# Optimization experiments

Hardware: AMD Instinct MI355X
Metric: run time of the kernel (lower is better)

The kernel has to match this reference:

```python
import jax, jax.numpy as jnp
import numpy as np

BS, D = 8192, 1024


def setup_inputs() -> dict:
    key = jax.random.key(0)
    k1, k2, k3, k4 = jax.random.split(key, 4)
    return {
        "z": jax.random.normal(k1, (BS, D), dtype=jnp.float32),
        "w": jax.random.normal(k2, (BS, D), dtype=jnp.float32),
        "u": jax.random.normal(k3, (BS, D), dtype=jnp.float32),
        "b": jax.random.normal(k4, (BS,), dtype=jnp.float32),
    }


def reference(z, w, u, b):
    # --- get_batch_corrected_u ---
    wu = jnp.sum(w * u, axis=1)                      # [bs]
    m = -1.0 + jax.nn.softplus(wu)                   # [bs]
    # NOTE: original divides by sqrt of GLOBAL sum over all of w (no axis)
    w_norm = jnp.sqrt(jnp.sum(w ** 2))               # scalar
    u_hat = u + ((m - wu)[:, None] * w) / w_norm     # [bs, d]

    # --- forward transform: diag(tanh(wTz+b)) @ u  ==  tanh(...)[:,None]*u ---
    inner = jnp.sum(w * z, axis=1) + b               # [bs]
    z_new = z + jnp.tanh(inner)[:, None] * u_hat     # [bs, d]

    # --- det_jcb evaluated with UPDATED z (as in the original code) ---
    inner2 = jnp.sum(w * z_new, axis=1) + b          # [bs]
    h_prime = 1.0 - jnp.tanh(inner2) ** 2            # [bs]
    psi_dot_u = h_prime * jnp.sum(u_hat * w, axis=1) # [bs]
    log_det = jnp.log(jnp.abs(1.0 + psi_dot_u))      # [bs]
    return z_new, log_det
```

## Files before the change

kernel.cpp:

```cpp
#include <hip/hip_runtime.h>
#include <math.h>

#define BS   8192
#define D    1024
#define NBLK 512
#define RPB  16
#define F4R  4

typedef float floatx4 __attribute__((ext_vector_type(4)));
typedef unsigned long long u64;

__global__ __launch_bounds__(512, 4) void planar512(
    const float* __restrict__ z, const float* __restrict__ w,
    const float* __restrict__ u, const float* __restrict__ b,
    float* __restrict__ zout, float* __restrict__ ldout,
    u64* __restrict__ slots, unsigned int* __restrict__ epoch)
{
    const int t    = threadIdx.x;
    const int wv   = t >> 6;
    const int l    = t & 63;
    const int row0 = blockIdx.x * RPB + wv * 2;

    const unsigned int e1 =
        __hip_atomic_load(epoch, __ATOMIC_RELAXED, __HIP_MEMORY_SCOPE_AGENT)
        + 1u;

    float4 wr[2][F4R];
    float  w2_s[2];
    float  w2acc = 0.f;
#pragma unroll
    for (int r = 0; r < 2; ++r) {
        const float4* w4 = (const float4*)w + (size_t)(row0 + r) * (D / 4);
        float w2 = 0.f;
#pragma unroll
        for (int k = 0; k < F4R; ++k) {
            const float4 a = w4[l + (k << 6)];
            wr[r][k] = a;
            w2 += a.x*a.x + a.y*a.y + a.z*a.z + a.w*a.w;
        }
#pragma unroll
        for (int off = 32; off > 0; off >>= 1) w2 += __shfl_xor(w2, off, 64);
        w2_s[r] = w2;
        w2acc  += w2;
    }
    float brow[2];
#pragma unroll
    for (int r = 0; r < 2; ++r) brow[r] = b[row0 + r];

    __shared__ float sw[8], sg[8];
    if (l == 0) sw[wv] = w2acc;
    __syncthreads();
    if (t == 0) {
        float p = 0.f;
#pragma unroll
        for (int i = 0; i < 8; ++i) p += sw[i];
        const u64 word = ((u64)e1 << 32) | (u64)__float_as_uint(p);
        __hip_atomic_store(&slots[blockIdx.x], word, __ATOMIC_RELAXED,
                           __HIP_MEMORY_SCOPE_AGENT);
    }

    float4 vr[2][F4R];
    float  wu_s[2], in_s[2], th_s[2];
#pragma unroll
    for (int r = 0; r < 2; ++r) {
        const int row = row0 + r;
        const float4* z4 = (const float4*)z + (size_t)row * (D / 4);
        const float4* u4 = (const float4*)u + (size_t)row * (D / 4);
        float4 zv[F4R], uv[F4R];
#pragma unroll
        for (int k = 0; k < F4R; ++k) {
            zv[k] = z4[l + (k << 6)];
            uv[k] = u4[l + (k << 6)];
        }
        float wu = 0.f, wz = 0.f;
#pragma unroll
        for (int k = 0; k < F4R; ++k) {
            const float4 a = wr[r][k];
            wu += a.x*uv[k].x + a.y*uv[k].y + a.z*uv[k].z + a.w*uv[k].w;
            wz += a.x*zv[k].x + a.y*zv[k].y + a.z*zv[k].z + a.w*zv[k].w;
        }
#pragma unroll
        for (int off = 32; off > 0; off >>= 1) {
            wu += __shfl_xor(wu, off, 64);
            wz += __shfl_xor(wz, off, 64);
        }
        const float inner = wz + brow[r];
        const float tnh   = tanhf(inner);
#pragma unroll
        for (int k = 0; k < F4R; ++k) {
            vr[r][k].x = fmaf(tnh, uv[k].x, zv[k].x);
            vr[r][k].y = fmaf(tnh, uv[k].y, zv[k].y);
            vr[r][k].z = fmaf(tnh, uv[k].z, zv[k].z);
            vr[r][k].w = fmaf(tnh, uv[k].w, zv[k].w);
        }
        wu_s[r] = wu; in_s[r] = inner; th_s[r] = tnh;
    }

    u64 a0;
    for (;;) {
        a0 = __hip_atomic_load(&slots[t], __ATOMIC_RELAXED,
                               __HIP_MEMORY_SCOPE_AGENT);
        if ((unsigned int)(a0 >> 32) == e1) break;
        __builtin_amdgcn_s_sleep(4);
    }
    float gs = __uint_as_float((unsigned int)a0);
#pragma unroll
    for (int off = 32; off > 0; off >>= 1) gs += __shfl_xor(gs, off, 64);
    if (l == 0) sg[wv] = gs;
    __syncthreads();
    float gw2 = 0.f;
#pragma unroll
    for (int i = 0; i < 8; ++i) gw2 += sg[i];
    const float wnrm = sqrtf(gw2);

    if (blockIdx.x == 0 && t == 0)
        __hip_atomic_store(epoch, e1, __ATOMIC_RELEASE,
                           __HIP_MEMORY_SCOPE_AGENT);

#pragma unroll
    for (int r = 0; r < 2; ++r) {
        const int   row  = row0 + r;
        const float wu   = wu_s[r];
        const float sp   = (wu > 0.f) ? (wu + log1pf(expf(-wu)))
                                      : log1pf(expf(wu));
        const float coef = (-1.f + sp - wu) / wnrm;
        const float tc   = th_s[r] * coef;
        floatx4* o4 = (floatx4*)zout + (size_t)row * (D / 4);
#pragma unroll
        for (int k = 0; k < F4R; ++k) {
            floatx4 o;
            o.x = fmaf(tc, wr[r][k].x, vr[r][k].x);
            o.y = fmaf(tc, wr[r][k].y, vr[r][k].y);
            o.z = fmaf(tc, wr[r][k].z, vr[r][k].z);
            o.w = fmaf(tc, wr[r][k].w, vr[r][k].w);
            __builtin_nontemporal_store(o, o4 + l + (k << 6));
        }
        if (l == 0) {
            const float s      = fmaf(coef, w2_s[r], wu);
            const float inner2 = fmaf(th_s[r], s, in_s[r]);
            const float th2    = tanhf(inner2);
            const float hp     = 1.f - th2 * th2;
            ldout[row] = logf(fabsf(fmaf(hp, s, 1.f)));
        }
    }
}

__global__ __launch_bounds__(256, 2) void planar256(
    const float* __restrict__ z, const float* __restrict__ w,
    const float* __restrict__ u, const float* __restrict__ b,
    float* __restrict__ zout, float* __restrict__ ldout,
    u64* __restrict__ slots, unsigned int* __restrict__ epoch)
{
    const int t    = threadIdx.x;
    const int wv   = t >> 6;
    const int l    = t & 63;
    const int row0 = blockIdx.x * RPB + wv * 4;

    __shared__ unsigned int s_e;
    __shared__ float sw[4], sg[4];
    if (t == 0)
        s_e = __hip_atomic_load(epoch, __ATOMIC_RELAXED,
                                __HIP_MEMORY_SCOPE_AGENT);

    float4 wr[4][F4R];
    float  w2_s[4];
    float  w2acc = 0.f;
#pragma unroll
    for (int r = 0; r < 4; ++r) {
        const float4* w4 = (const float4*)w + (size_t)(row0 + r) * (D / 4);
        float w2 = 0.f;
#pragma unroll
        for (int k = 0; k < F4R; ++k) {
            const float4 a = w4[l + (k << 6)];
            wr[r][k] = a;
            w2 += a.x*a.x + a.y*a.y + a.z*a.z + a.w*a.w;
        }
#pragma unroll
        for (int off = 32; off > 0; off >>= 1) w2 += __shfl_xor(w2, off, 64);
        w2_s[r] = w2;
        w2acc  += w2;
    }
    if (l == 0) sw[wv] = w2acc;
    __syncthreads();
    const unsigned int e1 = s_e + 1u;
    if (t == 0) {
        const float p = sw[0] + sw[1] + sw[2] + sw[3];
        const u64 word = ((u64)e1 << 32) | (u64)__float_as_uint(p);
        __hip_atomic_store(&slots[blockIdx.x], word, __ATOMIC_RELAXED,
                           __HIP_MEMORY_SCOPE_AGENT);
    }

    float4 vr[4][F4R];
    float  wu_s[4], in_s[4], th_s[4];
#pragma unroll
    for (int r = 0; r < 4; ++r) {
        const int row = row0 + r;
        const float4* z4 = (const float4*)z + (size_t)row * (D / 4);
        const float4* u4 = (const float4*)u + (size_t)row * (D / 4);
        float4 zv[F4R], uv[F4R];
#pragma unroll
        for (int k = 0; k < F4R; ++k) {
            zv[k] = z4[l + (k << 6)];
            uv[k] = u4[l + (k << 6)];
        }
        float wu = 0.f, wz = 0.f;
#pragma unroll
        for (int k = 0; k < F4R; ++k) {
            const float4 a = wr[r][k];
            wu += a.x*uv[k].x + a.y*uv[k].y + a.z*uv[k].z + a.w*uv[k].w;
            wz += a.x*zv[k].x + a.y*zv[k].y + a.z*zv[k].z + a.w*zv[k].w;
        }
#pragma unroll
        for (int off = 32; off > 0; off >>= 1) {
            wu += __shfl_xor(wu, off, 64);
            wz += __shfl_xor(wz, off, 64);
        }
        const float inner = wz + b[row];
        const float tnh   = tanhf(inner);
#pragma unroll
        for (int k = 0; k < F4R; ++k) {
            vr[r][k].x = fmaf(tnh, uv[k].x, zv[k].x);
            vr[r][k].y = fmaf(tnh, uv[k].y, zv[k].y);
            vr[r][k].z = fmaf(tnh, uv[k].z, zv[k].z);
            vr[r][k].w = fmaf(tnh, uv[k].w, zv[k].w);
        }
        wu_s[r] = wu; in_s[r] = inner; th_s[r] = tnh;
    }

    u64 a0, a1;
    for (;;) {
        a0 = __hip_atomic_load(&slots[t], __ATOMIC_RELAXED,
                               __HIP_MEMORY_SCOPE_AGENT);
        a1 = __hip_atomic_load(&slots[t + 256], __ATOMIC_RELAXED,
                               __HIP_MEMORY_SCOPE_AGENT);
        if ((unsigned int)(a0 >> 32) == e1 &&
            (unsigned int)(a1 >> 32) == e1) break;
        __builtin_amdgcn_s_sleep(4);
    }
    float gs = __uint_as_float((unsigned int)a0)
             + __uint_as_float((unsigned int)a1);
#pragma unroll
    for (int off = 32; off > 0; off >>= 1) gs += __shfl_xor(gs, off, 64);
    if (l == 0) sg[wv] = gs;
    __syncthreads();
    const float wnrm = sqrtf(sg[0] + sg[1] + sg[2] + sg[3]);

    if (blockIdx.x == 0 && t == 0)
        __hip_atomic_store(epoch, e1, __ATOMIC_RELEASE,
                           __HIP_MEMORY_SCOPE_AGENT);

#pragma unroll
    for (int r = 0; r < 4; ++r) {
        const int   row  = row0 + r;
        const float wu   = wu_s[r];
        const float sp   = (wu > 0.f) ? (wu + log1pf(expf(-wu)))
                                      : log1pf(expf(wu));
        const float coef = (-1.f + sp - wu) / wnrm;
        const float tc   = th_s[r] * coef;
        floatx4* o4 = (floatx4*)zout + (size_t)row * (D / 4);
#pragma unroll
        for (int k = 0; k < F4R; ++k) {
            floatx4 o;
            o.x = fmaf(tc, wr[r][k].x, vr[r][k].x);
            o.y = fmaf(tc, wr[r][k].y, vr[r][k].y);
            o.z = fmaf(tc, wr[r][k].z, vr[r][k].z);
            o.w = fmaf(tc, wr[r][k].w, vr[r][k].w);
            __builtin_nontemporal_store(o, o4 + l + (k << 6));
        }
        if (l == 0) {
            const float s      = fmaf(coef, w2_s[r], wu);
            const float inner2 = fmaf(th_s[r], s, in_s[r]);
            const float th2    = tanhf(inner2);
            const float hp     = 1.f - th2 * th2;
            ldout[row] = logf(fabsf(fmaf(hp, s, 1.f)));
        }
    }
}

extern "C" void kernel_launch(void* const* d_in, const int* in_sizes, int n_in,
                              void* d_out, int out_size, void* d_ws, size_t ws_size,
                              hipStream_t stream) {
    const float* z = (const float*)d_in[0];
    const float* w = (const float*)d_in[1];
    const float* u = (const float*)d_in[2];
    const float* b = (const float*)d_in[3];

    float* out   = (float*)d_out;
    float* zout  = out;
    float* ldout = out + (size_t)BS * D;

    u64*          slots = (u64*)d_ws;
    unsigned int* epoch = (unsigned int*)(slots + NBLK);

    int nb2 = 0;
    hipError_t err =
        hipOccupancyMaxActiveBlocksPerMultiprocessor(&nb2, planar512, 512, 0);
    if (err == hipSuccess && nb2 >= 2) {
        planar512<<<NBLK, 512, 0, stream>>>(z, w, u, b, zout, ldout,
                                            slots, epoch);
    } else {
        planar256<<<NBLK, 256, 0, stream>>>(z, w, u, b, zout, ldout,
                                            slots, epoch);
    }
}
```

Before: 25.14 us.

## Defer second row's z/u loads past grid barrier and poll slots per wave

The 512-thread kernel now processes only the first row before the grid-wide norm barrier and issues the second row's z/u loads after it, with sched_barriers pinning that order. The intent is to cut register pressure and spread memory traffic across the barrier wait. Each wave now polls all 512 slots itself and reduces them with shuffles, which drops the shared-memory exchange and the second __syncthreads. In exchange, the second row's load latency now sits after the barrier and slot polling traffic grows eightfold.

```diff
diff --git a/kernel.cpp b/kernel.cpp
--- a/kernel.cpp
+++ b/kernel.cpp
@@ -47,7 +47,7 @@
 #pragma unroll
     for (int r = 0; r < 2; ++r) brow[r] = b[row0 + r];
 
-    __shared__ float sw[8], sg[8];
+    __shared__ float sw[8];
     if (l == 0) sw[wv] = w2acc;
     __syncthreads();
     if (t == 0) {
@@ -59,13 +59,11 @@
                            __HIP_MEMORY_SCOPE_AGENT);
     }
 
-    float4 vr[2][F4R];
-    float  wu_s[2], in_s[2], th_s[2];
-#pragma unroll
-    for (int r = 0; r < 2; ++r) {
-        const int row = row0 + r;
-        const float4* z4 = (const float4*)z + (size_t)row * (D / 4);
-        const float4* u4 = (const float4*)u + (size_t)row * (D / 4);
+    float4 va[F4R];
+    float  wuA, inA, thA;
+    {
+        const float4* z4 = (const float4*)z + (size_t)row0 * (D / 4);
+        const float4* u4 = (const float4*)u + (size_t)row0 * (D / 4);
         float4 zv[F4R], uv[F4R];
 #pragma unroll
         for (int k = 0; k < F4R; ++k) {
@@ -75,7 +73,7 @@
         float wu = 0.f, wz = 0.f;
 #pragma unroll
         for (int k = 0; k < F4R; ++k) {
-            const float4 a = wr[r][k];
+            const float4 a = wr[0][k];
             wu += a.x*uv[k].x + a.y*uv[k].y + a.z*uv[k].z + a.w*uv[k].w;
             wz += a.x*zv[k].x + a.y*zv[k].y + a.z*zv[k].z + a.w*zv[k].w;
         }
@@ -84,60 +82,113 @@
             wu += __shfl_xor(wu, off, 64);
             wz += __shfl_xor(wz, off, 64);
         }
-        const float inner = wz + brow[r];
-        const float tnh   = tanhf(inner);
-#pragma unroll
-        for (int k = 0; k < F4R; ++k) {
-            vr[r][k].x = fmaf(tnh, uv[k].x, zv[k].x);
-            vr[r][k].y = fmaf(tnh, uv[k].y, zv[k].y);
-            vr[r][k].z = fmaf(tnh, uv[k].z, zv[k].z);
-            vr[r][k].w = fmaf(tnh, uv[k].w, zv[k].w);
-        }
-        wu_s[r] = wu; in_s[r] = inner; th_s[r] = tnh;
-    }
-
-    u64 a0;
+        inA = wz + brow[0];
+        thA = tanhf(inA);
+#pragma unroll
+        for (int k = 0; k < F4R; ++k) {
+            va[k].x = fmaf(thA, uv[k].x, zv[k].x);
+            va[k].y = fmaf(thA, uv[k].y, zv[k].y);
+            va[k].z = fmaf(thA, uv[k].z, zv[k].z);
+            va[k].w = fmaf(thA, uv[k].w, zv[k].w);
+        }
+        wuA = wu;
+    }
+
+    u64 a[8];
     for (;;) {
-        a0 = __hip_atomic_load(&slots[t], __ATOMIC_RELAXED,
-                               __HIP_MEMORY_SCOPE_AGENT);
-        if ((unsigned int)(a0 >> 32) == e1) break;
+        bool ok = true;
+#pragma unroll
+        for (int i = 0; i < 8; ++i) {
+            a[i] = __hip_atomic_load(&slots[l + (i << 6)], __ATOMIC_RELAXED,
+                                     __HIP_MEMORY_SCOPE_AGENT);
+            ok = ok && ((unsigned int)(a[i] >> 32) == e1);
+        }
+        if (__all(ok)) break;
         __builtin_amdgcn_s_sleep(4);
     }
-    float gs = __uint_as_float((unsigned int)a0);
+    float gs = 0.f;
+#pragma unroll
+    for (int i = 0; i < 8; ++i) gs += __uint_as_float((unsigned int)a[i]);
 #pragma unroll
     for (int off = 32; off > 0; off >>= 1) gs += __shfl_xor(gs, off, 64);
-    if (l == 0) sg[wv] = gs;
-    __syncthreads();
-    float gw2 = 0.f;
-#pragma unroll
-    for (int i = 0; i < 8; ++i) gw2 += sg[i];
-    const float wnrm = sqrtf(gw2);
+    const float wnrm = sqrtf(gs);
 
     if (blockIdx.x == 0 && t == 0)
         __hip_atomic_store(epoch, e1, __ATOMIC_RELEASE,
                            __HIP_MEMORY_SCOPE_AGENT);
 
-#pragma unroll
-    for (int r = 0; r < 2; ++r) {
-        const int   row  = row0 + r;
-        const float wu   = wu_s[r];
-        const float sp   = (wu > 0.f) ? (wu + log1pf(expf(-wu)))
-                                      : log1pf(expf(wu));
-        const float coef = (-1.f + sp - wu) / wnrm;
-        const float tc   = th_s[r] * coef;
+    __builtin_amdgcn_sched_barrier(0);
+
+    float4 zB[F4R], uB[F4R];
+    {
+        const float4* z4 = (const float4*)z + (size_t)(row0 + 1) * (D / 4);
+        const float4* u4 = (const float4*)u + (size_t)(row0 + 1) * (D / 4);
+#pragma unroll
+        for (int k = 0; k < F4R; ++k) {
+            zB[k] = z4[l + (k << 6)];
+            uB[k] = u4[l + (k << 6)];
+        }
+    }
+
+    __builtin_amdgcn_sched_barrier(0);
+
+    {
+        const float sp   = (wuA > 0.f) ? (wuA + log1pf(expf(-wuA)))
+                                       : log1pf(expf(wuA));
+        const float coef = (-1.f + sp - wuA) / wnrm;
+        const float tc   = thA * coef;
+        floatx4* o4 = (floatx4*)zout + (size_t)row0 * (D / 4);
+#pragma unroll
+        for (int k = 0; k < F4R; ++k) {
+            floatx4 o;
+            o.x = fmaf(tc, wr[0][k].x, va[k].x);
+            o.y = fmaf(tc, wr[0][k].y, va[k].y);
+            o.z = fmaf(tc, wr[0][k].z, va[k].z);
+            o.w = fmaf(tc, wr[0][k].w, va[k].w);
+            __builtin_nontemporal_store(o, o4 + l + (k << 6));
+        }
+        if (l == 0) {
+            const float s      = fmaf(coef, w2_s[0], wuA);
+            const float inner2 = fmaf(thA, s, inA);
+            const float th2    = tanhf(inner2);
+            const float hp     = 1.f - th2 * th2;
+            ldout[row0] = logf(fabsf(fmaf(hp, s, 1.f)));
+        }
+    }
+
+    {
+        const int row = row0 + 1;
+        float wu = 0.f, wz = 0.f;
+#pragma unroll
+        for (int k = 0; k < F4R; ++k) {
+            const float4 aa = wr[1][k];
+            wu += aa.x*uB[k].x + aa.y*uB[k].y + aa.z*uB[k].z + aa.w*uB[k].w;
+            wz += aa.x*zB[k].x + aa.y*zB[k].y + aa.z*zB[k].z + aa.w*zB[k].w;
+        }
+#pragma unroll
+        for (int off = 32; off > 0; off >>= 1) {
+            wu += __shfl_xor(wu, off, 64);
+            wz += __shfl_xor(wz, off, 64);
+        }
+        const float inner = wz + brow[1];
+        const float tnh   = tanhf(inner);
+        const float sp    = (wu > 0.f) ? (wu + log1pf(expf(-wu)))
+                                       : log1pf(expf(wu));
+        const float coef  = (-1.f + sp - wu) / wnrm;
+        const float tc    = tnh * coef;
         floatx4* o4 = (floatx4*)zout + (size_t)row * (D / 4);
 #pragma unroll
         for (int k = 0; k < F4R; ++k) {
             floatx4 o;
-            o.x = fmaf(tc, wr[r][k].x, vr[r][k].x);
-            o.y = fmaf(tc, wr[r][k].y, vr[r][k].y);
-            o.z = fmaf(tc, wr[r][k].z, vr[r][k].z);
-            o.w = fmaf(tc, wr[r][k].w, vr[r][k].w);
+            o.x = fmaf(tc, wr[1][k].x, fmaf(tnh, uB[k].x, zB[k].x));
+            o.y = fmaf(tc, wr[1][k].y, fmaf(tnh, uB[k].y, zB[k].y));
+            o.z = fmaf(tc, wr[1][k].z, fmaf(tnh, uB[k].z, zB[k].z));
+            o.w = fmaf(tc, wr[1][k].w, fmaf(tnh, uB[k].w, zB[k].w));
             __builtin_nontemporal_store(o, o4 + l + (k << 6));
         }
         if (l == 0) {
-            const float s      = fmaf(coef, w2_s[r], wu);
-            const float inner2 = fmaf(th_s[r], s, in_s[r]);
+            const float s      = fmaf(coef, w2_s[1], wu);
+            const float inner2 = fmaf(tnh, s, inner);
             const float th2    = tanhf(inner2);
             const float hp     = 1.f - th2 * th2;
             ldout[row] = logf(fabsf(fmaf(hp, s, 1.f)));
```

Result: no change. 25.08 us (-0.3%).
